# Optimization experiments

Measured on AMD Instinct MI355X. Metric: run time of the kernel, lower is better.

The kernel has to match this reference:

```python
import jax, jax.numpy as jnp
import numpy as np

N_NODES = 16384   # dim_size (number of aggregation groups)
DEG = 16          # neighbors per node
H = 128           # hidden_dim
E = N_NODES * DEG # total neighbor rows


def setup_inputs() -> dict:
    key = jax.random.key(0)
    k1, k2, k3 = jax.random.split(key, 3)
    x = jax.random.normal(k1, (E, H), dtype=jnp.float32)
    # sorted segment ids, DEG neighbors per node (ragged in general; uniform here)
    index = jnp.repeat(jnp.arange(N_NODES, dtype=jnp.int32), DEG)
    # torch LSTM params: gates stacked [i, f, g, o] -> [4H, H]
    W_ih = jax.random.normal(k2, (4 * H, H), dtype=jnp.float32) * 0.02  # xavier gain=0.02 scale
    W_hh = jax.random.normal(k3, (4 * H, H), dtype=jnp.float32) * (1.0 / np.sqrt(H))
    b_ih = jnp.zeros((4 * H,), jnp.float32)
    b_hh = jnp.zeros((4 * H,), jnp.float32)
    return {"x": x, "index": index, "W_ih": W_ih, "W_hh": W_hh,
            "b_ih": b_ih, "b_hh": b_hh, "dim_size": N_NODES}


def reference(x, index, W_ih, W_hh, b_ih, b_hh, dim_size):
    # Faithful to LSTMAggregator.forward: per-group gather of neighbor rows,
    # single-layer LSTM over each group's sequence, final hidden state h_n
    # written to out[group]; empty groups stay zero. (The original's randperm
    # shuffle is nondeterministic and omitted: neighbors kept in index order.)
    x = jnp.nan_to_num(x, nan=0.0)
    E_, Hd = x.shape

    # --- pack ragged groups into a padded [N, L, H] tensor ---
    order = jnp.argsort(index, stable=True)
    idx_s = index[order]
    counts = jax.ops.segment_sum(jnp.ones((E_,), jnp.int32), idx_s, num_segments=dim_size)
    starts = jnp.cumsum(counts) - counts           # exclusive prefix sum
    pos = jnp.arange(E_, dtype=jnp.int32) - starts[idx_s]  # position within group
    L = int(jnp.max(counts))                       # static at call time (concrete inputs)

    x_s = x[order]
    padded = jnp.zeros((dim_size, L, Hd), x.dtype).at[idx_s, pos].set(x_s)  # [N, L, H]
    valid = jnp.arange(L)[None, :] < counts[:, None]                        # [N, L]

    # --- batched masked LSTM scan over time ---
    bias = b_ih + b_hh
    h0 = jnp.zeros((dim_size, Hd), x.dtype)

    def step(carry, inp):
        h, c = carry
        xt, m = inp                                 # xt: [N, H], m: [N]
        gates = xt @ W_ih.T + h @ W_hh.T + bias     # [N, 4H], gate order i,f,g,o
        i, f, g, o = jnp.split(gates, 4, axis=-1)
        i = jax.nn.sigmoid(i); f = jax.nn.sigmoid(f)
        g = jnp.tanh(g);       o = jax.nn.sigmoid(o)
        c_new = f * c + i * g
        h_new = o * jnp.tanh(c_new)
        m = m[:, None]
        return (jnp.where(m, h_new, h), jnp.where(m, c_new, c)), None

    xs = (jnp.swapaxes(padded, 0, 1), valid.T)      # time-major [L, N, H], [L, N]
    (h_final, _), _ = jax.lax.scan(step, (h0, h0), xs)
    return jnp.nan_to_num(h_final, nan=0.0)        # [dim_size, H]
```

## Files before the change

### kernel.cpp

```cpp
#include <hip/hip_runtime.h>

#define DEG      16
#define HDIM     128
#define MB       32
#define NTHREADS 512

typedef __attribute__((ext_vector_type(8))) short  short8;
typedef __attribute__((ext_vector_type(4))) float  floatx4;
typedef __attribute__((ext_vector_type(4))) unsigned int uintx4;

#define MFMA(A,B,C) __builtin_amdgcn_mfma_f32_16x16x32_bf16(A,B,C,0,0,0)

__device__ __forceinline__ unsigned short f2bf(float f) {
  union { float f; unsigned int u; } v; v.f = f;
  unsigned int u = v.u;
  u += 0x7fffu + ((u >> 16) & 1u);
  return (unsigned short)(u >> 16);
}

__device__ __forceinline__ unsigned int cvtpk(float lo, float hi) {
  unsigned int r;
  asm("v_cvt_pk_bf16_f32 %0, %1, %2" : "=v"(r) : "v"(lo), "v"(hi));
  return r;
}

__device__ __forceinline__ float fsig(float x) {
  return __builtin_amdgcn_rcpf(1.0f + __expf(-x));
}
__device__ __forceinline__ float ftanh(float x) {
  return 1.0f - 2.0f * __builtin_amdgcn_rcpf(1.0f + __expf(2.0f * x));
}

__global__ void convert_w_kernel(const float* __restrict__ Wih,
                                 const float* __restrict__ Whh,
                                 unsigned short* __restrict__ Wsw) {
  int i    = blockIdx.x * 256 + threadIdx.x;
  int lane = i & 63;
  int frag = i >> 6;
  int kt = frag >> 5;
  int wg = frag & 31;
  int w  = wg >> 2;
  int g  = wg & 3;
  int j  = g * 128 + w * 16 + (lane & 15);
  int k0 = kt * 32 + (lane >> 4) * 8;
  const float* src = (k0 < HDIM) ? (Wih + (size_t)j * HDIM + k0)
                                 : (Whh + (size_t)j * HDIM + (k0 - HDIM));
  short8 o;
  #pragma unroll
  for (int e = 0; e < 8; ++e) o[e] = (short)f2bf(src[e]);
  *(short8*)(Wsw + (size_t)i * 8) = o;
}

#define ACT_X(MT, PAR, ACCP, ACCQ, LAST_, CS)                                  \
  {                                                                            \
    float hv[4];                                                               \
    _Pragma("unroll")                                                          \
    for (int r = 0; r < 4; ++r) {                                              \
      float iv = fsig (ACCP[0][MT][r]);                                        \
      float fv = fsig (ACCP[1][MT][r]);                                        \
      float gv = ftanh(ACCP[2][MT][r]);                                        \
      float ov = fsig (ACCP[3][MT][r]);                                        \
      float cn = fv * CS[r] + iv * gv;                                         \
      CS[r] = cn;                                                              \
      hv[r] = ov * ftanh(cn);                                                  \
    }                                                                          \
    if (LAST_) {                                                               \
      float* ob = out + (size_t)(node0 + MT * 16 + q * 4) * HDIM + j_g;        \
      _Pragma("unroll")                                                        \
      for (int r = 0; r < 4; ++r) ob[r * HDIM] = hv[r];                        \
    } else {                                                                   \
      unsigned int p01 = cvtpk(hv[0], hv[1]);                                  \
      unsigned int p23 = cvtpk(hv[2], hv[3]);                                  \
      *(unsigned short*)(hwp[0] + ((PAR ^ 1) * 8192 + MT * 4096)) = (unsigned short)p01;         \
      *(unsigned short*)(hwp[1] + ((PAR ^ 1) * 8192 + MT * 4096)) = (unsigned short)(p01 >> 16); \
      *(unsigned short*)(hwp[2] + ((PAR ^ 1) * 8192 + MT * 4096)) = (unsigned short)p23;         \
      *(unsigned short*)(hwp[3] + ((PAR ^ 1) * 8192 + MT * 4096)) = (unsigned short)(p23 >> 16); \
            \
      short8 ax0 = *(const short8*)(xsE + (PAR ^ 1) * 8192 + MT * 4096 + 0);   \
      short8 ax1 = *(const short8*)(xsO + (PAR ^ 1) * 8192 + MT * 4096 + 64);  \
      short8 ax2 = *(const short8*)(xsE + (PAR ^ 1) * 8192 + MT * 4096 + 128); \
      short8 ax3 = *(const short8*)(xsO + (PAR ^ 1) * 8192 + MT * 4096 + 192); \
      short8 w2[4];                                                            \
      _Pragma("unroll")                                                        \
      for (int g = 0; g < 4; ++g) w2[g] = *(const short8*)(wlB + g * 1024);    \
      _Pragma("unroll")                                                        \
      for (int g = 0; g < 4; ++g) {                                            \
        floatx4 bv = {bias[g], bias[g], bias[g], bias[g]};                     \
        floatx4 t0 = MFMA(ax0, breg[0][g], bv);                                \
        t0 = MFMA(ax1, breg[1][g], t0);                                        \
        t0 = MFMA(ax2, w2[g], t0);                                             \
        ACCQ[g][MT] = MFMA(ax3, b3[g], t0);                                    \
      }                                                                        \
    }                                                                          \
  }

#define STEP(T, PAR, ACCP, ACCQ, WITH_H, LAST_)                                \
  {                                                                            \
    const unsigned short* Wp = Wsw;                                            \
    asm volatile("" : "+s"(Wp));                     \
    if (WITH_H) {                                                              \
      _Pragma("unroll")                                                        \
      for (int kh = 0; kh < 4; ++kh) {                                         \
        const unsigned short* Wk = Wp + ((size_t)((4 + kh) * 32 + w_id * 4) * 64 + lane) * 8; \
        short8 bfr[4];                                                         \
        _Pragma("unroll")                                                      \
        for (int g = 0; g < 4; ++g) bfr[g] = *(const short8*)(Wk + g * 512);   \
        const char* hb = (kh & 1) ? hsO : hsE;                                 \
        short8 ah0 = *(const short8*)(hb + PAR * 8192 + 0    + kh * 64);       \
        short8 ah1 = *(const short8*)(hb + PAR * 8192 + 4096 + kh * 64);       \
        _Pragma("unroll")                                                      \
        for (int g = 0; g < 4; ++g) {                                          \
          ACCP[g][0] = MFMA(ah0, bfr[g], ACCP[g][0]);                          \
          ACCP[g][1] = MFMA(ah1, bfr[g], ACCP[g][1]);                          \
        }                                                                      \
      }                                                                        \
    }                                                                          \
    short8 b3[4];                                                              \
    if (!LAST_) {                                                              \
      const unsigned short* W3 = Wp + ((size_t)(96 + w_id * 4) * 64 + lane) * 8; \
      _Pragma("unroll")                                                        \
      for (int g = 0; g < 4; ++g) b3[g] = *(const short8*)(W3 + g * 512);      \
    }                                                                          \
    ACT_X(0, PAR, ACCP, ACCQ, LAST_, cs0)                                      \
    ACT_X(1, PAR, ACCP, ACCQ, LAST_, cs1)                                      \
    if (!LAST_ && (T) + 2 < DEG) {                                             \
      uintx4 p;                                                                \
      p[0] = cvtpk(xp0[0], xp0[1]); p[1] = cvtpk(xp0[2], xp0[3]);              \
      p[2] = cvtpk(xp1[0], xp1[1]); p[3] = cvtpk(xp1[2], xp1[3]);              \
      *(uintx4*)(xsW + PAR * 8192) = p;                                        \
      if ((T) + 3 < DEG) {                                                     \
        const float* xq_ = xb0 + (size_t)((T) + 3) * HDIM;                     \
        xp0 = ((const floatx4*)xq_)[0]; xp1 = ((const floatx4*)xq_)[1];        \
      }                                                                        \
    }                                                                          \
    __syncthreads();                                                           \
  }

__global__ __launch_bounds__(NTHREADS, 2)
void lstm_agg_kernel(const float* __restrict__ x,
                     const float* __restrict__ b_ih,
                     const float* __restrict__ b_hh,
                     const unsigned short* __restrict__ Wsw,
                     float* __restrict__ out) {
  __shared__ __align__(16) unsigned short Xs[2 * MB * HDIM];
  __shared__ __align__(16) unsigned short Hs[2 * MB * HDIM];
  __shared__ __align__(16) unsigned short Wl[32 * 512];

  const int tid  = threadIdx.x;
  const int w_id = tid >> 6;
  const int lane = tid & 63;
  const int l15  = lane & 15;
  const int q    = lane >> 4;
  const int node0 = blockIdx.x * MB;
  const int j_g = w_id * 16 + l15;

  float bias[4];
  #pragma unroll
  for (int g = 0; g < 4; ++g) bias[g] = b_ih[g * 128 + j_g] + b_hh[g * 128 + j_g];

  short8 breg[2][4];
  #pragma unroll
  for (int kt = 0; kt < 2; ++kt)
    #pragma unroll
    for (int g = 0; g < 4; ++g) {
      int fi = kt * 32 + w_id * 4 + g;
      breg[kt][g] = *(const short8*)(Wsw + ((size_t)fi * 64 + lane) * 8);
    }

  #pragma unroll
  for (int i = 0; i < 4; ++i) {
    int o = tid * 32 + i * 8;
    *(short8*)&Wl[o] = *(const short8*)(Wsw + 2 * 32 * 512 + o);
  }

  const int fA  = (l15 & 7) ^ ((l15 & 8) >> 2);
  const int qx  = (q ^ (fA & 3)) << 4;
  const int f64 = (fA >> 2) << 6;
  const char* xsE = (const char*)Xs + l15 * 256 + qx + f64;
  const char* xsO = (const char*)Xs + l15 * 256 + qx - f64;
  const char* hsE = (const char*)Hs + l15 * 256 + qx + f64;
  const char* hsO = (const char*)Hs + l15 * 256 + qx - f64;

  const char* wlB = (const char*)Wl + w_id * 4096 + lane * 16;

  const int hc  = j_g >> 3;
  const int hkl = j_g & 7;
  char* hwp[4];
  #pragma unroll
  for (int r = 0; r < 4; ++r) {
    int m  = q * 4 + r;
    int fr = (m & 7) ^ ((m & 8) >> 2);
    hwp[r] = (char*)Hs + m * 256 + ((hc ^ fr) << 4) + hkl * 2;
  }

  const int m_x = tid >> 4;
  const int kc  = tid & 15;
  const int fX  = (m_x & 7) ^ ((m_x & 8) >> 2);
  const float* xb0 = x + ((size_t)(node0 + m_x) * DEG) * HDIM + kc * 8;
  char* xsW = (char*)Xs + m_x * 256 + ((kc ^ fX) << 4);

  floatx4 cs0 = {0.f, 0.f, 0.f, 0.f};
  floatx4 cs1 = {0.f, 0.f, 0.f, 0.f};
  floatx4 accA[4][2], accB[4][2];
  floatx4 xp0, xp1;

  {
    floatx4 u0 = ((const floatx4*)xb0)[0], u1 = ((const floatx4*)xb0)[1];
    uintx4 p;
    p[0] = cvtpk(u0[0], u0[1]); p[1] = cvtpk(u0[2], u0[3]);
    p[2] = cvtpk(u1[0], u1[1]); p[3] = cvtpk(u1[2], u1[3]);
    *(uintx4*)xsW = p;
    u0 = ((const floatx4*)(xb0 + HDIM))[0]; u1 = ((const floatx4*)(xb0 + HDIM))[1];
    p[0] = cvtpk(u0[0], u0[1]); p[1] = cvtpk(u0[2], u0[3]);
    p[2] = cvtpk(u1[0], u1[1]); p[3] = cvtpk(u1[2], u1[3]);
    *(uintx4*)(xsW + 8192) = p;
    xp0 = ((const floatx4*)(xb0 + 2 * HDIM))[0];
    xp1 = ((const floatx4*)(xb0 + 2 * HDIM))[1];
  }
  __syncthreads();

  {
    short8 b3p[4];
    const unsigned short* W3 = Wsw + ((size_t)(96 + w_id * 4) * 64 + lane) * 8;
    #pragma unroll
    for (int g = 0; g < 4; ++g) b3p[g] = *(const short8*)(W3 + g * 512);
    #pragma unroll
    for (int mt = 0; mt < 2; ++mt) {
      short8 ax0 = *(const short8*)(xsE + mt * 4096 + 0);
      short8 ax1 = *(const short8*)(xsO + mt * 4096 + 64);
      short8 ax2 = *(const short8*)(xsE + mt * 4096 + 128);
      short8 ax3 = *(const short8*)(xsO + mt * 4096 + 192);
      short8 w2[4];
      #pragma unroll
      for (int g = 0; g < 4; ++g) w2[g] = *(const short8*)(wlB + g * 1024);
      #pragma unroll
      for (int g = 0; g < 4; ++g) {
        floatx4 bv = {bias[g], bias[g], bias[g], bias[g]};
        floatx4 t0 = MFMA(ax0, breg[0][g], bv);
        t0 = MFMA(ax1, breg[1][g], t0);
        t0 = MFMA(ax2, w2[g], t0);
        accA[g][mt] = MFMA(ax3, b3p[g], t0);
      }
    }
  }
  __syncthreads();

  STEP(0, 0, accA, accB, 0, 0)
  #pragma unroll 1
  for (int t = 1; t < 15; t += 2) {
    STEP(t,     1, accB, accA, 1, 0)
    STEP(t + 1, 0, accA, accB, 1, 0)
  }
  STEP(15, 1, accB, accA, 1, 1)
}

extern "C" void kernel_launch(void* const* d_in, const int* in_sizes, int n_in,
                              void* d_out, int out_size, void* d_ws, size_t ws_size,
                              hipStream_t stream) {
  const float* x   = (const float*)d_in[0];
  const float* Wih = (const float*)d_in[2];
  const float* Whh = (const float*)d_in[3];
  const float* bih = (const float*)d_in[4];
  const float* bhh = (const float*)d_in[5];
  unsigned short* Wsw = (unsigned short*)d_ws;
  float* out = (float*)d_out;

  hipLaunchKernelGGL(convert_w_kernel, dim3(64), dim3(256), 0, stream, Wih, Whh, Wsw);

  int nodes   = in_sizes[0] / (DEG * HDIM);
  int nblocks = nodes / MB;
  hipLaunchKernelGGL(lstm_agg_kernel, dim3(nblocks), dim3(NTHREADS), 0, stream,
                     x, bih, bhh, Wsw, out);
}
```

Baseline: 262.0 us.

## Fold log2e into weights, single accumulator set, raise occupancy to 4 blocks/CU

Pre-scales the gate weights and biases by log2(e) (2·log2(e) for the tanh gate) so the activations can use a raw exp2 instead of exp. Drops the double-buffered accA/accB accumulators and the register-resident x-weight fragments. The x-projection now runs after the activation, reading its weights from global or LDS each step, and launch bounds rise from 2 to 4 blocks per CU. The aim is lower register pressure for more occupancy and fewer VALU ops in the activations, at the cost of more weight loads per step and less overlap between the activations and the MFMAs.

```diff
diff --git a/kernel.cpp b/kernel.cpp
--- a/kernel.cpp
+++ b/kernel.cpp
@@ -10,6 +10,8 @@
 typedef __attribute__((ext_vector_type(4))) unsigned int uintx4;
 
 #define MFMA(A,B,C) __builtin_amdgcn_mfma_f32_16x16x32_bf16(A,B,C,0,0,0)
+#define L2E  1.4426950408889634f
+#define L2E2 2.8853900817779268f
 
 __device__ __forceinline__ unsigned short f2bf(float f) {
   union { float f; unsigned int u; } v; v.f = f;
@@ -24,11 +26,20 @@
   return r;
 }
 
-__device__ __forceinline__ float fsig(float x) {
-  return __builtin_amdgcn_rcpf(1.0f + __expf(-x));
-}
-__device__ __forceinline__ float ftanh(float x) {
-  return 1.0f - 2.0f * __builtin_amdgcn_rcpf(1.0f + __expf(2.0f * x));
+#if __has_builtin(__builtin_amdgcn_exp2f)
+#define FEXP2(x) __builtin_amdgcn_exp2f(x)
+#else
+__device__ __forceinline__ float FEXP2_fn(float x) {
+  float r; asm("v_exp_f32 %0, %1" : "=v"(r) : "v"(x)); return r;
+}
+#define FEXP2(x) FEXP2_fn(x)
+#endif
+
+__device__ __forceinline__ float fsig2(float s) {
+  return __builtin_amdgcn_rcpf(1.0f + FEXP2(-s));
+}
+__device__ __forceinline__ float ftanh2(float s) {
+  return 1.0f - 2.0f * __builtin_amdgcn_rcpf(1.0f + FEXP2(s));
 }
 
 __global__ void convert_w_kernel(const float* __restrict__ Wih,
@@ -43,100 +54,134 @@
   int g  = wg & 3;
   int j  = g * 128 + w * 16 + (lane & 15);
   int k0 = kt * 32 + (lane >> 4) * 8;
+  float sc = (g == 2) ? L2E2 : L2E;
   const float* src = (k0 < HDIM) ? (Wih + (size_t)j * HDIM + k0)
                                  : (Whh + (size_t)j * HDIM + (k0 - HDIM));
   short8 o;
   #pragma unroll
-  for (int e = 0; e < 8; ++e) o[e] = (short)f2bf(src[e]);
+  for (int e = 0; e < 8; ++e) o[e] = (short)f2bf(src[e] * sc);
   *(short8*)(Wsw + (size_t)i * 8) = o;
 }
 
-#define ACT_X(MT, PAR, ACCP, ACCQ, LAST_, CS)                                  \
+
+#define HPART(HOFF)                                                            \
+  {                                                                            \
+    const unsigned short* Wp = Wsw;                                            \
+    asm volatile("" : "+s"(Wp));                     \
+    _Pragma("unroll")                                                          \
+    for (int kh = 0; kh < 4; ++kh) {                                           \
+      const unsigned short* Wk = Wp + ((size_t)((4 + kh) * 32 + w_id * 4) * 64 + lane) * 8; \
+      short8 bfr[4];                                                           \
+      _Pragma("unroll")                                                        \
+      for (int g = 0; g < 4; ++g) bfr[g] = *(const short8*)(Wk + g * 512);     \
+      const char* hb = (kh & 1) ? hsO : hsE;                                   \
+      short8 ah0 = *(const short8*)(hb + (HOFF) + 0    + kh * 64);             \
+      short8 ah1 = *(const short8*)(hb + (HOFF) + 4096 + kh * 64);             \
+      _Pragma("unroll")                                                        \
+      for (int g = 0; g < 4; ++g) {                                            \
+        acc[g][0] = MFMA(ah0, bfr[g], acc[g][0]);                              \
+        acc[g][1] = MFMA(ah1, bfr[g], acc[g][1]);                              \
+      }                                                                        \
+    }                                                                          \
+  }
+
+#define ACT1(MT, WOFF, LAST_, CS)                                              \
   {                                                                            \
     float hv[4];                                                               \
     _Pragma("unroll")                                                          \
     for (int r = 0; r < 4; ++r) {                                              \
-      float iv = fsig (ACCP[0][MT][r]);                                        \
-      float fv = fsig (ACCP[1][MT][r]);                                        \
-      float gv = ftanh(ACCP[2][MT][r]);                                        \
-      float ov = fsig (ACCP[3][MT][r]);                                        \
+      float iv = fsig2 (acc[0][MT][r]);                                        \
+      float fv = fsig2 (acc[1][MT][r]);                                        \
+      float gv = ftanh2(acc[2][MT][r]);                                        \
+      float ov = fsig2 (acc[3][MT][r]);                                        \
       float cn = fv * CS[r] + iv * gv;                                         \
       CS[r] = cn;                                                              \
-      hv[r] = ov * ftanh(cn);                                                  \
+      hv[r] = ov * ftanh2(L2E2 * cn);                                          \
     }                                                                          \
     if (LAST_) {                                                               \
-      float* ob = out + (size_t)(node0 + MT * 16 + q * 4) * HDIM + j_g;        \
+      float* ob = out + (size_t)(node0 + (MT) * 16 + q * 4) * HDIM + j_g;      \
       _Pragma("unroll")                                                        \
       for (int r = 0; r < 4; ++r) ob[r * HDIM] = hv[r];                        \
     } else {                                                                   \
       unsigned int p01 = cvtpk(hv[0], hv[1]);                                  \
       unsigned int p23 = cvtpk(hv[2], hv[3]);                                  \
-      *(unsigned short*)(hwp[0] + ((PAR ^ 1) * 8192 + MT * 4096)) = (unsigned short)p01;         \
-      *(unsigned short*)(hwp[1] + ((PAR ^ 1) * 8192 + MT * 4096)) = (unsigned short)(p01 >> 16); \
-      *(unsigned short*)(hwp[2] + ((PAR ^ 1) * 8192 + MT * 4096)) = (unsigned short)p23;         \
-      *(unsigned short*)(hwp[3] + ((PAR ^ 1) * 8192 + MT * 4096)) = (unsigned short)(p23 >> 16); \
-            \
-      short8 ax0 = *(const short8*)(xsE + (PAR ^ 1) * 8192 + MT * 4096 + 0);   \
-      short8 ax1 = *(const short8*)(xsO + (PAR ^ 1) * 8192 + MT * 4096 + 64);  \
-      short8 ax2 = *(const short8*)(xsE + (PAR ^ 1) * 8192 + MT * 4096 + 128); \
-      short8 ax3 = *(const short8*)(xsO + (PAR ^ 1) * 8192 + MT * 4096 + 192); \
-      short8 w2[4];                                                            \
-      _Pragma("unroll")                                                        \
-      for (int g = 0; g < 4; ++g) w2[g] = *(const short8*)(wlB + g * 1024);    \
-      _Pragma("unroll")                                                        \
-      for (int g = 0; g < 4; ++g) {                                            \
-        floatx4 bv = {bias[g], bias[g], bias[g], bias[g]};                     \
-        floatx4 t0 = MFMA(ax0, breg[0][g], bv);                                \
-        t0 = MFMA(ax1, breg[1][g], t0);                                        \
-        t0 = MFMA(ax2, w2[g], t0);                                             \
-        ACCQ[g][MT] = MFMA(ax3, b3[g], t0);                                    \
-      }                                                                        \
-    }                                                                          \
-  }
-
-#define STEP(T, PAR, ACCP, ACCQ, WITH_H, LAST_)                                \
+      *(unsigned short*)(hwp[0] + (WOFF) + (MT) * 4096) = (unsigned short)p01;         \
+      *(unsigned short*)(hwp[1] + (WOFF) + (MT) * 4096) = (unsigned short)(p01 >> 16); \
+      *(unsigned short*)(hwp[2] + (WOFF) + (MT) * 4096) = (unsigned short)p23;         \
+      *(unsigned short*)(hwp[3] + (WOFF) + (MT) * 4096) = (unsigned short)(p23 >> 16); \
+    }                                                                          \
+  }
+
+#define XPART(XOFF)                                                            \
   {                                                                            \
     const unsigned short* Wp = Wsw;                                            \
-    asm volatile("" : "+s"(Wp));                     \
-    if (WITH_H) {                                                              \
-      _Pragma("unroll")                                                        \
-      for (int kh = 0; kh < 4; ++kh) {                                         \
-        const unsigned short* Wk = Wp + ((size_t)((4 + kh) * 32 + w_id * 4) * 64 + lane) * 8; \
-        short8 bfr[4];                                                         \
-        _Pragma("unroll")                                                      \
-        for (int g = 0; g < 4; ++g) bfr[g] = *(const short8*)(Wk + g * 512);   \
-        const char* hb = (kh & 1) ? hsO : hsE;                                 \
-        short8 ah0 = *(const short8*)(hb + PAR * 8192 + 0    + kh * 64);       \
-        short8 ah1 = *(const short8*)(hb + PAR * 8192 + 4096 + kh * 64);       \
-        _Pragma("unroll")                                                      \
-        for (int g = 0; g < 4; ++g) {                                          \
-          ACCP[g][0] = MFMA(ah0, bfr[g], ACCP[g][0]);                          \
-          ACCP[g][1] = MFMA(ah1, bfr[g], ACCP[g][1]);                          \
+    asm volatile("" : "+s"(Wp));                                               \
+    const unsigned short* Wx = Wp + ((size_t)(w_id * 256 + lane)) * 8;         \
+    short8 wv[4]; short8 a0, a1;                                               \
+                                    \
+    _Pragma("unroll")                                                          \
+    for (int g = 0; g < 4; ++g) wv[g] = *(const short8*)(Wx + g * 512);        \
+    a0 = *(const short8*)(xsE + (XOFF) + 0);                                   \
+    a1 = *(const short8*)(xsE + (XOFF) + 4096 + 0);                            \
+    _Pragma("unroll")                                                          \
+    for (int g = 0; g < 4; ++g) {                                              \
+      acc[g][0] = MFMA(a0, wv[g], bias4[g]);                                   \
+      acc[g][1] = MFMA(a1, wv[g], bias4[g]);                                   \
+    }                                                                          \
+                                                                 \
+    _Pragma("unroll")                                                          \
+    for (int g = 0; g < 4; ++g) wv[g] = *(const short8*)(Wx + 16384 + g * 512);\
+    a0 = *(const short8*)(xsO + (XOFF) + 64);                                  \
+    a1 = *(const short8*)(xsO + (XOFF) + 4096 + 64);                           \
+    _Pragma("unroll")                                                          \
+    for (int g = 0; g < 4; ++g) {                                              \
+      acc[g][0] = MFMA(a0, wv[g], acc[g][0]);                                  \
+      acc[g][1] = MFMA(a1, wv[g], acc[g][1]);                                  \
+    }                                                                          \
+                                                                \
+    _Pragma("unroll")                                                          \
+    for (int g = 0; g < 4; ++g) wv[g] = *(const short8*)(wlB + g * 1024);      \
+    a0 = *(const short8*)(xsE + (XOFF) + 128);                                 \
+    a1 = *(const short8*)(xsE + (XOFF) + 4096 + 128);                          \
+    _Pragma("unroll")                                                          \
+    for (int g = 0; g < 4; ++g) {                                              \
+      acc[g][0] = MFMA(a0, wv[g], acc[g][0]);                                  \
+      acc[g][1] = MFMA(a1, wv[g], acc[g][1]);                                  \
+    }                                                                          \
+                                                                 \
+    _Pragma("unroll")                                                          \
+    for (int g = 0; g < 4; ++g) wv[g] = *(const short8*)(Wx + 49152 + g * 512);\
+    a0 = *(const short8*)(xsO + (XOFF) + 192);                                 \
+    a1 = *(const short8*)(xsO + (XOFF) + 4096 + 192);                          \
+    _Pragma("unroll")                                                          \
+    for (int g = 0; g < 4; ++g) {                                              \
+      acc[g][0] = MFMA(a0, wv[g], acc[g][0]);                                  \
+      acc[g][1] = MFMA(a1, wv[g], acc[g][1]);                                  \
+    }                                                                          \
+  }
+
+#define STEP(T, PAR, WITH_H, LAST_)                                            \
+  {                                                                            \
+    if (WITH_H) HPART((PAR) * 8192);                                           \
+    ACT1(0, ((PAR) ^ 1) * 8192, LAST_, cs0)                                    \
+    ACT1(1, ((PAR) ^ 1) * 8192, LAST_, cs1)                                    \
+    if (!(LAST_)) {                                                            \
+      XPART((((PAR) ^ 1)) * 8192)                                              \
+      if ((T) + 2 < DEG) {                                                     \
+        uintx4 p;                                                              \
+        p[0] = cvtpk(xp0[0], xp0[1]); p[1] = cvtpk(xp0[2], xp0[3]);            \
+        p[2] = cvtpk(xp1[0], xp1[1]); p[3] = cvtpk(xp1[2], xp1[3]);            \
+        *(uintx4*)(xsW + (PAR) * 8192) = p;                                    \
+        if ((T) + 3 < DEG) {                                                   \
+          const float* xq_ = xb0 + (size_t)((T) + 3) * HDIM;                   \
+          xp0 = ((const floatx4*)xq_)[0]; xp1 = ((const floatx4*)xq_)[1];      \
         }                                                                      \
       }                                                                        \
     }                                                                          \
-    short8 b3[4];                                                              \
-    if (!LAST_) {                                                              \
-      const unsigned short* W3 = Wp + ((size_t)(96 + w_id * 4) * 64 + lane) * 8; \
-      _Pragma("unroll")                                                        \
-      for (int g = 0; g < 4; ++g) b3[g] = *(const short8*)(W3 + g * 512);      \
-    }                                                                          \
-    ACT_X(0, PAR, ACCP, ACCQ, LAST_, cs0)                                      \
-    ACT_X(1, PAR, ACCP, ACCQ, LAST_, cs1)                                      \
-    if (!LAST_ && (T) + 2 < DEG) {                                             \
-      uintx4 p;                                                                \
-      p[0] = cvtpk(xp0[0], xp0[1]); p[1] = cvtpk(xp0[2], xp0[3]);              \
-      p[2] = cvtpk(xp1[0], xp1[1]); p[3] = cvtpk(xp1[2], xp1[3]);              \
-      *(uintx4*)(xsW + PAR * 8192) = p;                                        \
-      if ((T) + 3 < DEG) {                                                     \
-        const float* xq_ = xb0 + (size_t)((T) + 3) * HDIM;                     \
-        xp0 = ((const floatx4*)xq_)[0]; xp1 = ((const floatx4*)xq_)[1];        \
-      }                                                                        \
-    }                                                                          \
     __syncthreads();                                                           \
   }
 
-__global__ __launch_bounds__(NTHREADS, 2)
+__global__ __launch_bounds__(NTHREADS, 4)
 void lstm_agg_kernel(const float* __restrict__ x,
                      const float* __restrict__ b_ih,
                      const float* __restrict__ b_hh,
@@ -154,18 +199,13 @@
   const int node0 = blockIdx.x * MB;
   const int j_g = w_id * 16 + l15;
 
-  float bias[4];
-  #pragma unroll
-  for (int g = 0; g < 4; ++g) bias[g] = b_ih[g * 128 + j_g] + b_hh[g * 128 + j_g];
-
-  short8 breg[2][4];
-  #pragma unroll
-  for (int kt = 0; kt < 2; ++kt)
-    #pragma unroll
-    for (int g = 0; g < 4; ++g) {
-      int fi = kt * 32 + w_id * 4 + g;
-      breg[kt][g] = *(const short8*)(Wsw + ((size_t)fi * 64 + lane) * 8);
-    }
+  floatx4 bias4[4];
+  #pragma unroll
+  for (int g = 0; g < 4; ++g) {
+    float b = (b_ih[g * 128 + j_g] + b_hh[g * 128 + j_g]) * ((g == 2) ? L2E2 : L2E);
+    floatx4 bv = {b, b, b, b};
+    bias4[g] = bv;
+  }
 
   #pragma unroll
   for (int i = 0; i < 4; ++i) {
@@ -201,7 +241,7 @@
 
   floatx4 cs0 = {0.f, 0.f, 0.f, 0.f};
   floatx4 cs1 = {0.f, 0.f, 0.f, 0.f};
-  floatx4 accA[4][2], accB[4][2];
+  floatx4 acc[4][2];
   floatx4 xp0, xp1;
 
   {
@@ -219,39 +259,16 @@
   }
   __syncthreads();
 
-  {
-    short8 b3p[4];
-    const unsigned short* W3 = Wsw + ((size_t)(96 + w_id * 4) * 64 + lane) * 8;
-    #pragma unroll
-    for (int g = 0; g < 4; ++g) b3p[g] = *(const short8*)(W3 + g * 512);
-    #pragma unroll
-    for (int mt = 0; mt < 2; ++mt) {
-      short8 ax0 = *(const short8*)(xsE + mt * 4096 + 0);
-      short8 ax1 = *(const short8*)(xsO + mt * 4096 + 64);
-      short8 ax2 = *(const short8*)(xsE + mt * 4096 + 128);
-      short8 ax3 = *(const short8*)(xsO + mt * 4096 + 192);
-      short8 w2[4];
-      #pragma unroll
-      for (int g = 0; g < 4; ++g) w2[g] = *(const short8*)(wlB + g * 1024);
-      #pragma unroll
-      for (int g = 0; g < 4; ++g) {
-        floatx4 bv = {bias[g], bias[g], bias[g], bias[g]};
-        floatx4 t0 = MFMA(ax0, breg[0][g], bv);
-        t0 = MFMA(ax1, breg[1][g], t0);
-        t0 = MFMA(ax2, w2[g], t0);
-        accA[g][mt] = MFMA(ax3, b3p[g], t0);
-      }
-    }
-  }
+  XPART(0)
   __syncthreads();
 
-  STEP(0, 0, accA, accB, 0, 0)
+  STEP(0, 0, 0, 0)
   #pragma unroll 1
   for (int t = 1; t < 15; t += 2) {
-    STEP(t,     1, accB, accA, 1, 0)
-    STEP(t + 1, 0, accA, accB, 1, 0)
-  }
-  STEP(15, 1, accB, accA, 1, 1)
+    STEP(t,     1, 1, 0)
+    STEP(t + 1, 0, 1, 0)
+  }
+  STEP(15, 1, 1, 1)
 }
 
 extern "C" void kernel_launch(void* const* d_in, const int* in_sizes, int n_in,
```

New measurement: 284.8 us. 1.09x slower.
